# Optimization experiments

Hardware: AMD Instinct MI355X
Metric: run time of the kernel (lower is better)

Reference implementation:

```python
import jax, jax.numpy as jnp
import numpy as np

EMBED_DIM = 400          # d; entity embedding is 2d (alpha|beta)
N_ENTITY = 100000
N_RELATION = 500
HIDDEN = 1600
BATCH = 8192


def _reg(x):
    # Regularizer(base_add=1, min_val=0.05, max_val=1e9)
    return jnp.clip(x + 1.0, 0.05, 1e9)


def setup_inputs() -> dict:
    key = jax.random.key(0)
    ks = jax.random.split(key, 16)
    d = EMBED_DIM
    rng = (9.0 + 2.0) / d  # (gamma + epsilon) / embed_dim with gamma=9

    def xavier(k, shape):
        fan_out, fan_in = shape
        lim = np.sqrt(6.0 / (fan_in + fan_out))
        return jax.random.uniform(k, shape, jnp.float32, -lim, lim)

    inp = {
        "anchor1_idx": jax.random.randint(ks[0], (BATCH,), 0, N_ENTITY),
        "rel1_idx": jax.random.randint(ks[1], (BATCH,), 0, N_RELATION),
        "anchor2_idx": jax.random.randint(ks[2], (BATCH,), 0, N_ENTITY),
        "rel2_idx": jax.random.randint(ks[3], (BATCH,), 0, N_RELATION),
        # embedding tables
        "entity_embedding": jax.random.uniform(ks[4], (N_ENTITY, 2 * d), jnp.float32, -rng, rng),
        "relation_embedding": jax.random.uniform(ks[5], (N_RELATION, d), jnp.float32, -rng, rng),
        # BetaProjection: layer1 [hidden, 2d+d], layer2 [hidden, hidden], layer0 [2d, hidden]
        "pW1": xavier(ks[6], (HIDDEN, 3 * d)),
        "pb1": jnp.zeros((HIDDEN,), jnp.float32),
        "pW2": xavier(ks[7], (HIDDEN, HIDDEN)),
        "pb2": jnp.zeros((HIDDEN,), jnp.float32),
        "pW0": xavier(ks[8], (2 * d, HIDDEN)),
        "pb0": jnp.zeros((2 * d,), jnp.float32),
        # BetaIntersection: layer1 [2d, 2d], layer2 [d, 2d]
        "iW1": xavier(ks[9], (2 * d, 2 * d)),
        "ib1": jnp.zeros((2 * d,), jnp.float32),
        "iW2": xavier(ks[10], (d, 2 * d)),
        "ib2": jnp.zeros((d,), jnp.float32),
    }
    return inp


def _projection(e_emb, r_emb, pW1, pb1, pW2, pb2, pW0, pb0):
    # cat -> Linear+ReLU (layer1) -> Linear+ReLU (layer2) -> layer0 -> regularizer
    x = jnp.concatenate([e_emb, r_emb], axis=-1)           # [B, 3d]
    x = jax.nn.relu(x @ pW1.T + pb1)                       # [B, H]
    x = jax.nn.relu(x @ pW2.T + pb2)                       # [B, H]
    x = x @ pW0.T + pb0                                    # [B, 2d]
    return _reg(x)


def _intersection(alphas, betas, iW1, ib1, iW2, ib2):
    # alphas/betas: [K, B, d]; softmax attention over K
    all_emb = jnp.concatenate([alphas, betas], axis=-1)    # [K, B, 2d]
    h = jax.nn.relu(all_emb @ iW1.T + ib1)                 # [K, B, 2d]
    att = jax.nn.softmax(h @ iW2.T + ib2, axis=0)          # [K, B, d]
    return jnp.sum(att * alphas, axis=0), jnp.sum(att * betas, axis=0)


def reference(anchor1_idx, rel1_idx, anchor2_idx, rel2_idx,
              entity_embedding, relation_embedding,
              pW1, pb1, pW2, pb2, pW0, pb0,
              iW1, ib1, iW2, ib2):
    h = _reg(entity_embedding)                             # entity_regularizer
    r = relation_embedding

    emb1 = _projection(h[anchor1_idx], r[rel1_idx], pW1, pb1, pW2, pb2, pW0, pb0)
    a1, b1 = jnp.split(emb1, 2, axis=-1)
    emb2 = _projection(h[anchor2_idx], r[rel2_idx], pW1, pb1, pW2, pb2, pW0, pb0)
    a2, b2 = jnp.split(emb2, 2, axis=-1)

    alpha, beta = _intersection(jnp.stack([a1, a2]), jnp.stack([b1, b2]),
                                iW1, ib1, iW2, ib2)
    return alpha, beta
```

## Files before the change

kernel.cpp:

```cpp
#include <hip/hip_runtime.h>
#include <hip/hip_bf16.h>
#include <stdint.h>

typedef __bf16 bf16_t;
typedef __bf16 bf16x8 __attribute__((ext_vector_type(8)));
typedef float f32x4 __attribute__((ext_vector_type(4)));

constexpr int BATCH = 8192;
constexpr int M = 2 * BATCH;

constexpr int K1 = 1216;
constexpr int LDC1 = 1664, NS1 = 1600;
constexpr int LDA2 = 1664, KL2 = 1600;
constexpr int LDC2 = 1664, NS2 = 1600;
constexpr int LDA3 = 1664, KL3 = 1600;
constexpr int N3c = 1024;
constexpr int LDC3 = 1024, NS3 = 832;
constexpr int LDA4 = 1024, KL4 = 832;
constexpr int N4c = 1024;
constexpr int LDC4 = 1024, NS4 = 832;
constexpr int LDA5 = 1024, KL5 = 832, N5 = 512;
constexpr int NW1 = 1792, NW2 = 1792;

__device__ __forceinline__ void gload_lds16(const void* g, void* l) {
  __builtin_amdgcn_global_load_lds(
      (const __attribute__((address_space(1))) void*)g,
      (__attribute__((address_space(3))) void*)l,
      16, 0, 0);
}

#define CFENCE() asm volatile("" ::: "memory")
#define BAR()  { CFENCE(); __builtin_amdgcn_s_barrier(); CFENCE(); }

__device__ __forceinline__ void doconv(int idx, const float* __restrict__ src,
                                       bf16_t* __restrict__ dst, int Nr, int Kc, int Kp) {
  const int kp4 = Kp >> 2;
  const int r = idx / kp4;
  const int c = (idx - r * kp4) << 2;
  union { bf16_t h[4]; uint2 u; } pk;
#pragma unroll
  for (int j = 0; j < 4; ++j) {
    const int cc = c + j;
    const float v = (r < Nr && cc < Kc) ? src[(size_t)r * Kc + cc] : 0.f;
    pk.h[j] = (bf16_t)v;
  }
  *(uint2*)(dst + (size_t)r * Kp + c) = pk.u;
}

constexpr int CJ0 = NW1 * K1 / 4;
constexpr int CJ1 = CJ0 + NW2 * LDA2 / 4;
constexpr int CJ2 = CJ1 + N3c * LDA3 / 4;
constexpr int CJ3 = CJ2 + N4c * LDA4 / 4;
constexpr int CJ4 = CJ3 + N5 * LDA5 / 4;
constexpr int GATHERB = 2048;
constexpr int CONVB = 2048;
constexpr int PREPB = GATHERB + CONVB;

__global__ void prep_kernel(const int* __restrict__ a1, const int* __restrict__ r1,
                            const int* __restrict__ a2, const int* __restrict__ r2,
                            const float* __restrict__ ent, const float* __restrict__ rel,
                            bf16_t* __restrict__ X,
                            const float* __restrict__ pW1, const float* __restrict__ pW2,
                            const float* __restrict__ pW0, const float* __restrict__ iW1,
                            const float* __restrict__ iW2,
                            bf16_t* __restrict__ W1b, bf16_t* __restrict__ W2b,
                            bf16_t* __restrict__ W0b, bf16_t* __restrict__ iW1b,
                            bf16_t* __restrict__ iW2b) {
  if (blockIdx.x < GATHERB) {
    for (int r8 = 0; r8 < 8; ++r8) {
      const int row = blockIdx.x * 8 + r8;
      const int b   = row & (BATCH - 1);
      const int br  = row >> 13;
      const int eidx = br ? a2[b] : a1[b];
      const int ridx = br ? r2[b] : r1[b];
      const float* __restrict__ esrc = ent + (size_t)eidx * 800;
      const float* __restrict__ rsrc = rel + (size_t)ridx * 400;
      bf16_t* __restrict__ dst = X + (size_t)row * K1;
      for (int g = threadIdx.x; g < K1 / 4; g += 256) {
        const int c = g * 4;
        float4 v = make_float4(0.f, 0.f, 0.f, 0.f);
        if (c < 800) {
          v = *(const float4*)(esrc + c);
          v.x = fminf(fmaxf(v.x + 1.f, 0.05f), 1e9f);
          v.y = fminf(fmaxf(v.y + 1.f, 0.05f), 1e9f);
          v.z = fminf(fmaxf(v.z + 1.f, 0.05f), 1e9f);
          v.w = fminf(fmaxf(v.w + 1.f, 0.05f), 1e9f);
        } else if (c < 1200) {
          v = *(const float4*)(rsrc + (c - 800));
        }
        union { bf16_t h[4]; uint2 u; } pk;
        pk.h[0] = (bf16_t)v.x; pk.h[1] = (bf16_t)v.y;
        pk.h[2] = (bf16_t)v.z; pk.h[3] = (bf16_t)v.w;
        *(uint2*)(dst + c) = pk.u;
      }
    }
  } else {
    for (int idx = (blockIdx.x - GATHERB) * 256 + threadIdx.x; idx < CJ4;
         idx += CONVB * 256) {
      if (idx < CJ0)      doconv(idx,        pW1, W1b, 1600, 1200, K1);
      else if (idx < CJ1) doconv(idx - CJ0,  pW2, W2b, 1600, 1600, LDA2);
      else if (idx < CJ2) doconv(idx - CJ1,  pW0, W0b,  800, 1600, LDA3);
      else if (idx < CJ3) doconv(idx - CJ2,  iW1, iW1b, 800,  800, LDA4);
      else                doconv(idx - CJ3,  iW2, iW2b, 400,  800, LDA5);
    }
  }
}

enum { ACT_RELU = 0, ACT_REG = 1 };

template <int ACT, int NFR>
__device__ __forceinline__
void gemm_body(const bf16_t* __restrict__ A, const bf16_t* __restrict__ Bw,
               const float* __restrict__ bias, int Nbias, bf16_t* __restrict__ Cb,
               int lda, int Nstore, int ldc, int NT, int bm, int col0,
               bf16_t* ldsbase, int t) {
  const int lane = t & 63;
  const int wv = t >> 6;
  const int wm = wv >> 2, wn = wv & 3;
  const int l15 = lane & 15;
  const int kbs = (((lane >> 4) ^ ((l15 >> 1) & 3)) << 4);

  const int srow = t >> 2;
  const int skc  = (t & 3) ^ ((t >> 3) & 3);
  const bf16_t* aR0 = A  + (size_t)(bm * 256 + srow) * lda + skc * 8;
  const bf16_t* aR1 = aR0 + (size_t)128 * lda;
  const bf16_t* bR0 = Bw + (size_t)(col0 + srow) * lda + skc * 8;
  const bf16_t* bR1 = bR0 + (size_t)128 * lda;
  const int ldsb0 = (wv * 64) * 16;
  const int ldsb1 = (512 + wv * 64) * 16;

  auto SLOT = [&](int s) { return ldsbase + s * 8192; };
  auto STAGE = [&](const bf16_t* r0p, const bf16_t* r1p, int kOff, bf16_t* slot) {
    gload_lds16(r0p + kOff, (char*)slot + ldsb0);
    gload_lds16(r1p + kOff, (char*)slot + ldsb1);
  };

  f32x4 acc[8][NFR];
#pragma unroll
  for (int i = 0; i < 8; ++i)
#pragma unroll
    for (int j = 0; j < NFR; ++j) acc[i][j] = f32x4{0.f, 0.f, 0.f, 0.f};

  STAGE(aR0, aR1, 0, SLOT(0));
  STAGE(bR0, bR1, 0, SLOT(2));
  STAGE(aR0, aR1, 32, SLOT(1));
  STAGE(bR0, bR1, 32, SLOT(3));
  if (NT > 1) {
    STAGE(aR0, aR1, 64, SLOT(4));
    STAGE(bR0, bR1, 64, SLOT(6));
    asm volatile("s_waitcnt vmcnt(8)" ::: "memory");
  } else {
    asm volatile("s_waitcnt vmcnt(4)" ::: "memory");
  }
  __builtin_amdgcn_s_barrier();
  CFENCE();

  bf16x8 bfr[NFR];
  int db = 0;
  for (int kt = 0; kt < NT; ++kt, db ^= 1) {
    const bool p1 = (kt + 1) < NT;
    const bool p2 = (kt + 2) < NT;
    bf16_t* const cur = SLOT(db * 4);
    bf16_t* const nxt = SLOT((db ^ 1) * 4);

    {
      const char* sA = (const char*)(cur);
      const char* sB = (const char*)(cur + 2 * 8192);
      bf16x8 af[4];
#pragma unroll
      for (int i = 0; i < 4; ++i)
        af[i] = *(const bf16x8*)(sA + ((wm * 128 + i * 16 + l15) << 6) + kbs);
#pragma unroll
      for (int i = 0; i < NFR; ++i)
        bfr[i] = *(const bf16x8*)(sB + ((wn * (NFR * 16) + i * 16 + l15) << 6) + kbs);
      if (p1) STAGE(aR0, aR1, (kt + 1) * 64 + 32, nxt + 1 * 8192);
      BAR();
      __builtin_amdgcn_s_setprio(1);
#pragma unroll
      for (int i = 0; i < 4; ++i)
#pragma unroll
        for (int j = 0; j < NFR; ++j)
          acc[i][j] = __builtin_amdgcn_mfma_f32_16x16x32_bf16(af[i], bfr[j], acc[i][j], 0, 0, 0);
      __builtin_amdgcn_s_setprio(0);
      BAR();
    }
    {
      const char* sA = (const char*)(cur);
      bf16x8 af[4];
#pragma unroll
      for (int i = 0; i < 4; ++i)
        af[i] = *(const bf16x8*)(sA + ((wm * 128 + (4 + i) * 16 + l15) << 6) + kbs);
      if (p1) STAGE(bR0, bR1, (kt + 1) * 64 + 32, nxt + 3 * 8192);
      BAR();
      __builtin_amdgcn_s_setprio(1);
#pragma unroll
      for (int i = 0; i < 4; ++i)
#pragma unroll
        for (int j = 0; j < NFR; ++j)
          acc[4 + i][j] = __builtin_amdgcn_mfma_f32_16x16x32_bf16(af[i], bfr[j], acc[4 + i][j], 0, 0, 0);
      __builtin_amdgcn_s_setprio(0);
      if (p1) asm volatile("s_waitcnt vmcnt(8)" ::: "memory");
      else    asm volatile("s_waitcnt vmcnt(0)" ::: "memory");
      BAR();
    }
    {
      const char* sA = (const char*)(cur + 1 * 8192);
      const char* sB = (const char*)(cur + 3 * 8192);
      bf16x8 af[4];
#pragma unroll
      for (int i = 0; i < 4; ++i)
        af[i] = *(const bf16x8*)(sA + ((wm * 128 + i * 16 + l15) << 6) + kbs);
#pragma unroll
      for (int i = 0; i < NFR; ++i)
        bfr[i] = *(const bf16x8*)(sB + ((wn * (NFR * 16) + i * 16 + l15) << 6) + kbs);
      if (p2) STAGE(aR0, aR1, (kt + 2) * 64, cur + 0 * 8192);
      BAR();
      __builtin_amdgcn_s_setprio(1);
#pragma unroll
      for (int i = 0; i < 4; ++i)
#pragma unroll
        for (int j = 0; j < NFR; ++j)
          acc[i][j] = __builtin_amdgcn_mfma_f32_16x16x32_bf16(af[i], bfr[j], acc[i][j], 0, 0, 0);
      __builtin_amdgcn_s_setprio(0);
      BAR();
    }
    {
      const char* sA = (const char*)(cur + 1 * 8192);
      bf16x8 af[4];
#pragma unroll
      for (int i = 0; i < 4; ++i)
        af[i] = *(const bf16x8*)(sA + ((wm * 128 + (4 + i) * 16 + l15) << 6) + kbs);
      if (p2) STAGE(bR0, bR1, (kt + 2) * 64, cur + 2 * 8192);
      BAR();
      __builtin_amdgcn_s_setprio(1);
#pragma unroll
      for (int i = 0; i < 4; ++i)
#pragma unroll
        for (int j = 0; j < NFR; ++j)
          acc[4 + i][j] = __builtin_amdgcn_mfma_f32_16x16x32_bf16(af[i], bfr[j], acc[4 + i][j], 0, 0, 0);
      __builtin_amdgcn_s_setprio(0);
      if (p1) {
        if (p2) asm volatile("s_waitcnt vmcnt(8)" ::: "memory");
        else    asm volatile("s_waitcnt vmcnt(4)" ::: "memory");
      }
      BAR();
    }
  }

  const int r0 = bm * 256 + wm * 128 + ((lane >> 4) * 4);
  const int c0 = col0 + wn * (NFR * 16) + l15;
#pragma unroll
  for (int ni = 0; ni < NFR; ++ni) {
    const int col = c0 + ni * 16;
    const float bv = (col < Nbias) ? bias[col] : 0.f;
    const bool cok = (col < Nstore);
#pragma unroll
    for (int mi = 0; mi < 8; ++mi) {
#pragma unroll
      for (int j = 0; j < 4; ++j) {
        float v = acc[mi][ni][j] + bv;
        if (ACT == ACT_RELU) v = fmaxf(v, 0.f);
        else                 v = fminf(fmaxf(v + 1.f, 0.05f), 1e9f);
        if (cok) Cb[(size_t)(r0 + mi * 16 + j) * ldc + col] = (bf16_t)v;
      }
    }
  }
}

template <int ACT, bool MIXED>
__global__ __launch_bounds__(512)
void gemm256(const bf16_t* __restrict__ A, const bf16_t* __restrict__ Bw,
             const float* __restrict__ bias, int Nbias,
             bf16_t* __restrict__ Cb,
             int lda, int Nstore, int ldc, int NT, int gridN) {
  __shared__ __align__(16) bf16_t lds[8][8192];
  const int nwg = gridDim.x;
  const int id = blockIdx.x;
  const int swz = (id & 7) * (nwg >> 3) + (id >> 3);
  const int bn = swz % gridN, bm = swz / gridN;
  const int t = threadIdx.x;
  if (MIXED) {
    const int col0 = bn * 192;
    if (bn < gridN - 1)
      gemm_body<ACT, 3>(A, Bw, bias, Nbias, Cb, lda, Nstore, ldc, NT, bm, col0, &lds[0][0], t);
    else
      gemm_body<ACT, 4>(A, Bw, bias, Nbias, Cb, lda, Nstore, ldc, NT, bm, col0, &lds[0][0], t);
  } else {
    gemm_body<ACT, 4>(A, Bw, bias, Nbias, Cb, lda, Nstore, ldc, NT, bm, bn * 256, &lds[0][0], t);
  }
}

constexpr int NT5 = KL5 / 64;
__global__ __launch_bounds__(256)
void g5_combine(const bf16_t* __restrict__ H, const bf16_t* __restrict__ Wb,
                const float* __restrict__ ib2, const bf16_t* __restrict__ E,
                float* __restrict__ out) {
  __shared__ __align__(16) bf16_t As1[2][8192];
  __shared__ __align__(16) bf16_t As2[2][8192];
  __shared__ __align__(16) bf16_t Bs[2][8192];

  const int bn = blockIdx.x, bm = blockIdx.y;
  const int t = threadIdx.x;
  const int lane = t & 63;
  const int wv = t >> 6;
  const int wm = wv >> 1, wn = wv & 1;

  f32x4 acc1[4][4], acc2[4][4];
#pragma unroll
  for (int i = 0; i < 4; ++i)
#pragma unroll
    for (int j = 0; j < 4; ++j) { acc1[i][j] = f32x4{0.f,0.f,0.f,0.f}; acc2[i][j] = f32x4{0.f,0.f,0.f,0.f}; }

  const size_t a1Base = (size_t)(bm * 128) * LDA5;
  const size_t a2Base = (size_t)(8192 + bm * 128) * LDA5;
  const size_t bBase  = (size_t)(bn * 128) * LDA5;

  auto stage = [&](int db, int kt) {
#pragma unroll
    for (int q = 0; q < 4; ++q) {
      const int lin = q * 256 + t;
      const int row = lin >> 3;
      const int kc = ((lin & 7) ^ (row & 7)) * 8;
      const int lofs = (q * 256 + wv * 64) * 16;
      gload_lds16(H + a1Base + (size_t)row * LDA5 + kt + kc, (char*)As1[db] + lofs);
      gload_lds16(H + a2Base + (size_t)row * LDA5 + kt + kc, (char*)As2[db] + lofs);
      gload_lds16(Wb + bBase + (size_t)row * LDA5 + kt + kc, (char*)Bs[db] + lofs);
    }
  };

  stage(0, 0);
  __syncthreads();
  int db = 0;
  for (int it = 0; it < NT5; ++it) {
    if (it + 1 < NT5) stage(db ^ 1, (it + 1) * 64);
#pragma unroll
    for (int s = 0; s < 2; ++s) {
      const int crd = s * 4 + (lane >> 4);
      const int k0 = (crd ^ (lane & 7)) * 8;
      bf16x8 af1[4], af2[4], bf[4];
#pragma unroll
      for (int i = 0; i < 4; ++i) {
        const int ra = wm * 64 + i * 16 + (lane & 15);
        af1[i] = *(const bf16x8*)(As1[db] + ra * 64 + k0);
        af2[i] = *(const bf16x8*)(As2[db] + ra * 64 + k0);
        const int rb = wn * 64 + i * 16 + (lane & 15);
        bf[i] = *(const bf16x8*)(Bs[db] + rb * 64 + k0);
      }
#pragma unroll
      for (int mi = 0; mi < 4; ++mi)
#pragma unroll
        for (int ni = 0; ni < 4; ++ni) {
          acc1[mi][ni] = __builtin_amdgcn_mfma_f32_16x16x32_bf16(af1[mi], bf[ni], acc1[mi][ni], 0, 0, 0);
          acc2[mi][ni] = __builtin_amdgcn_mfma_f32_16x16x32_bf16(af2[mi], bf[ni], acc2[mi][ni], 0, 0, 0);
        }
    }
    __syncthreads();
    db ^= 1;
  }

  const int rloc0 = wm * 64 + ((lane >> 4) * 4);
  const int cloc0 = wn * 64 + (lane & 15);
#pragma unroll
  for (int ni = 0; ni < 4; ++ni) {
    const int d = bn * 128 + cloc0 + ni * 16;
    if (d >= 400) continue;
    const float bv = ib2[d];
#pragma unroll
    for (int mi = 0; mi < 4; ++mi) {
#pragma unroll
      for (int j = 0; j < 4; ++j) {
        const int b = bm * 128 + rloc0 + mi * 16 + j;
        const float l1 = acc1[mi][ni][j] + bv;
        const float l2 = acc2[mi][ni][j] + bv;
        const float att1 = 1.f / (1.f + expf(l2 - l1));
        const float att2 = 1.f - att1;
        const bf16_t* E1 = E + (size_t)b * LDC3;
        const bf16_t* E2 = E + (size_t)(8192 + b) * LDC3;
        out[(size_t)b * 400 + d] =
            att1 * (float)E1[d] + att2 * (float)E2[d];
        out[(size_t)8192 * 400 + (size_t)b * 400 + d] =
            att1 * (float)E1[400 + d] + att2 * (float)E2[400 + d];
      }
    }
  }
}

extern "C" void kernel_launch(void* const* d_in, const int* in_sizes, int n_in,
                              void* d_out, int out_size, void* d_ws, size_t ws_size,
                              hipStream_t stream) {
  const int* a1 = (const int*)d_in[0];
  const int* r1 = (const int*)d_in[1];
  const int* a2 = (const int*)d_in[2];
  const int* r2 = (const int*)d_in[3];
  const float* ent = (const float*)d_in[4];
  const float* rel = (const float*)d_in[5];
  const float* pW1 = (const float*)d_in[6];
  const float* pb1 = (const float*)d_in[7];
  const float* pW2 = (const float*)d_in[8];
  const float* pb2 = (const float*)d_in[9];
  const float* pW0 = (const float*)d_in[10];
  const float* pb0 = (const float*)d_in[11];
  const float* iW1 = (const float*)d_in[12];
  const float* ib1 = (const float*)d_in[13];
  const float* iW2 = (const float*)d_in[14];
  const float* ib2 = (const float*)d_in[15];

  char* ws = (char*)d_ws;
  size_t o = 0;
  auto take = [&](size_t bytes) { char* p = ws + o; o += (bytes + 255) & ~(size_t)255; return p; };
  bf16_t* W1b  = (bf16_t*)take((size_t)NW1 * K1 * 2);
  bf16_t* W2b  = (bf16_t*)take((size_t)NW2 * LDA2 * 2);
  bf16_t* W0b  = (bf16_t*)take((size_t)N3c * LDA3 * 2);
  bf16_t* iW1b = (bf16_t*)take((size_t)N4c * LDA4 * 2);
  bf16_t* iW2b = (bf16_t*)take((size_t)N5 * LDA5 * 2);
  char* bufX = take((size_t)M * K1 * 2);
  char* bufY = take((size_t)M * LDC1 * 2);
  char* bufZ = take((size_t)M * LDC2 * 2);

  bf16_t* Xb = (bf16_t*)bufX;
  bf16_t* Yb = (bf16_t*)bufY;
  bf16_t* Zb = (bf16_t*)bufZ;
  bf16_t* Eb = (bf16_t*)bufX;
  bf16_t* Hb = (bf16_t*)bufY;

  prep_kernel<<<dim3(PREPB), 256, 0, stream>>>(a1, r1, a2, r2, ent, rel, Xb,
                                               pW1, pW2, pW0, iW1, iW2,
                                               W1b, W2b, W0b, iW1b, iW2b);

  gemm256<ACT_RELU, true><<<dim3(8 * (M / 256)), 512, 0, stream>>>(
      Xb, W1b, pb1, 1600, Yb, K1, NS1, LDC1, K1 / 64, 8);
  gemm256<ACT_RELU, true><<<dim3(8 * (M / 256)), 512, 0, stream>>>(
      Yb, W2b, pb2, 1600, Zb, LDA2, NS2, LDC2, KL2 / 64, 8);
  gemm256<ACT_REG, false><<<dim3(4 * (M / 256)), 512, 0, stream>>>(
      Zb, W0b, pb0, 800, Eb, LDA3, NS3, LDC3, KL3 / 64, 4);
  gemm256<ACT_RELU, false><<<dim3(4 * (M / 256)), 512, 0, stream>>>(
      Eb, iW1b, ib1, 800, Hb, LDA4, NS4, LDC4, KL4 / 64, 4);
  g5_combine<<<dim3(N5 / 128, BATCH / 128), 256, 0, stream>>>(
      Hb, iW2b, ib2, Eb, (float*)d_out);
}
```

Before: 349.0 us.

## Precompute relation-part of first projection layer as per-relation table

Splits the first projection GEMM into an entity part (K reduced from 1216 to 832) and a relation part. The relation part is computed once per distinct relation (500 rows) by a small GEMM into a table, then added in the epilogue through each row's relation index. The K of the largest-M first layer shrinks by about a third, at the cost of an extra small kernel and gathered bias-like loads in the epilogue. The first and second layer grids are also remapped with a fixed block-to-tile ordering.

```diff
diff --git a/kernel.cpp b/kernel.cpp
--- a/kernel.cpp
+++ b/kernel.cpp
@@ -9,7 +9,7 @@
 constexpr int BATCH = 8192;
 constexpr int M = 2 * BATCH;
 
-constexpr int K1 = 1216;
+constexpr int K1 = 832;
 constexpr int LDC1 = 1664, NS1 = 1600;
 constexpr int LDA2 = 1664, KL2 = 1600;
 constexpr int LDC2 = 1664, NS2 = 1600;
@@ -21,6 +21,8 @@
 constexpr int LDC4 = 1024, NS4 = 832;
 constexpr int LDA5 = 1024, KL5 = 832, N5 = 512;
 constexpr int NW1 = 1792, NW2 = 1792;
+constexpr int KREL = 448;
+constexpr int LDP = 1664;
 
 __device__ __forceinline__ void gload_lds16(const void* g, void* l) {
   __builtin_amdgcn_global_load_lds(
@@ -32,7 +34,7 @@
 #define CFENCE() asm volatile("" ::: "memory")
 #define BAR()  { CFENCE(); __builtin_amdgcn_s_barrier(); CFENCE(); }
 
-__device__ __forceinline__ void doconv(int idx, const float* __restrict__ src,
+__device__ __forceinline__ void doconv(int idx, const float* __restrict__ src, int sstride,
                                        bf16_t* __restrict__ dst, int Nr, int Kc, int Kp) {
   const int kp4 = Kp >> 2;
   const int r = idx / kp4;
@@ -41,7 +43,7 @@
 #pragma unroll
   for (int j = 0; j < 4; ++j) {
     const int cc = c + j;
-    const float v = (r < Nr && cc < Kc) ? src[(size_t)r * Kc + cc] : 0.f;
+    const float v = (r < Nr && cc < Kc) ? src[(size_t)r * sstride + cc] : 0.f;
     pk.h[j] = (bf16_t)v;
   }
   *(uint2*)(dst + (size_t)r * Kp + c) = pk.u;
@@ -52,6 +54,8 @@
 constexpr int CJ2 = CJ1 + N3c * LDA3 / 4;
 constexpr int CJ3 = CJ2 + N4c * LDA4 / 4;
 constexpr int CJ4 = CJ3 + N5 * LDA5 / 4;
+constexpr int CJ5 = CJ4 + LDP * KREL / 4;
+constexpr int CJ6 = CJ5 + 512 * KREL / 4;
 constexpr int GATHERB = 2048;
 constexpr int CONVB = 2048;
 constexpr int PREPB = GATHERB + CONVB;
@@ -59,13 +63,14 @@
 __global__ void prep_kernel(const int* __restrict__ a1, const int* __restrict__ r1,
                             const int* __restrict__ a2, const int* __restrict__ r2,
                             const float* __restrict__ ent, const float* __restrict__ rel,
-                            bf16_t* __restrict__ X,
+                            bf16_t* __restrict__ X, int* __restrict__ relrow,
                             const float* __restrict__ pW1, const float* __restrict__ pW2,
                             const float* __restrict__ pW0, const float* __restrict__ iW1,
                             const float* __restrict__ iW2,
-                            bf16_t* __restrict__ W1b, bf16_t* __restrict__ W2b,
+                            bf16_t* __restrict__ W1a, bf16_t* __restrict__ W2b,
                             bf16_t* __restrict__ W0b, bf16_t* __restrict__ iW1b,
-                            bf16_t* __restrict__ iW2b) {
+                            bf16_t* __restrict__ iW2b, bf16_t* __restrict__ W1bT,
+                            bf16_t* __restrict__ relbf) {
   if (blockIdx.x < GATHERB) {
     for (int r8 = 0; r8 < 8; ++r8) {
       const int row = blockIdx.x * 8 + r8;
@@ -73,8 +78,8 @@
       const int br  = row >> 13;
       const int eidx = br ? a2[b] : a1[b];
       const int ridx = br ? r2[b] : r1[b];
+      if (threadIdx.x == 0) relrow[row] = ridx;
       const float* __restrict__ esrc = ent + (size_t)eidx * 800;
-      const float* __restrict__ rsrc = rel + (size_t)ridx * 400;
       bf16_t* __restrict__ dst = X + (size_t)row * K1;
       for (int g = threadIdx.x; g < K1 / 4; g += 256) {
         const int c = g * 4;
@@ -85,8 +90,6 @@
           v.y = fminf(fmaxf(v.y + 1.f, 0.05f), 1e9f);
           v.z = fminf(fmaxf(v.z + 1.f, 0.05f), 1e9f);
           v.w = fminf(fmaxf(v.w + 1.f, 0.05f), 1e9f);
-        } else if (c < 1200) {
-          v = *(const float4*)(rsrc + (c - 800));
         }
         union { bf16_t h[4]; uint2 u; } pk;
         pk.h[0] = (bf16_t)v.x; pk.h[1] = (bf16_t)v.y;
@@ -95,24 +98,27 @@
       }
     }
   } else {
-    for (int idx = (blockIdx.x - GATHERB) * 256 + threadIdx.x; idx < CJ4;
+    for (int idx = (blockIdx.x - GATHERB) * 256 + threadIdx.x; idx < CJ6;
          idx += CONVB * 256) {
-      if (idx < CJ0)      doconv(idx,        pW1, W1b, 1600, 1200, K1);
-      else if (idx < CJ1) doconv(idx - CJ0,  pW2, W2b, 1600, 1600, LDA2);
-      else if (idx < CJ2) doconv(idx - CJ1,  pW0, W0b,  800, 1600, LDA3);
-      else if (idx < CJ3) doconv(idx - CJ2,  iW1, iW1b, 800,  800, LDA4);
-      else                doconv(idx - CJ3,  iW2, iW2b, 400,  800, LDA5);
-    }
-  }
-}
-
-enum { ACT_RELU = 0, ACT_REG = 1 };
-
-template <int ACT, int NFR>
+      if (idx < CJ0)      doconv(idx,        pW1, 1200, W1a, 1600,  800, K1);
+      else if (idx < CJ1) doconv(idx - CJ0,  pW2, 1600, W2b, 1600, 1600, LDA2);
+      else if (idx < CJ2) doconv(idx - CJ1,  pW0, 1600, W0b,  800, 1600, LDA3);
+      else if (idx < CJ3) doconv(idx - CJ2,  iW1,  800, iW1b, 800,  800, LDA4);
+      else if (idx < CJ4) doconv(idx - CJ3,  iW2,  800, iW2b, 400,  800, LDA5);
+      else if (idx < CJ5) doconv(idx - CJ4,  pW1 + 800, 1200, W1bT, 1600, 400, KREL);
+      else                doconv(idx - CJ5,  rel,  400, relbf, 500, 400, KREL);
+    }
+  }
+}
+
+enum { ACT_RELU = 0, ACT_REG = 1, ACT_NONE = 2 };
+
+template <int ACT, int NFR, bool ROWADD>
 __device__ __forceinline__
 void gemm_body(const bf16_t* __restrict__ A, const bf16_t* __restrict__ Bw,
                const float* __restrict__ bias, int Nbias, bf16_t* __restrict__ Cb,
                int lda, int Nstore, int ldc, int NT, int bm, int col0,
+               const int* __restrict__ relrow, const bf16_t* __restrict__ Pb,
                bf16_t* ldsbase, int t) {
   const int lane = t & 63;
   const int wv = t >> 6;
@@ -249,44 +255,130 @@
 
   const int r0 = bm * 256 + wm * 128 + ((lane >> 4) * 4);
   const int c0 = col0 + wn * (NFR * 16) + l15;
+  float bvv[NFR]; int colv[NFR]; bool cokv[NFR];
 #pragma unroll
   for (int ni = 0; ni < NFR; ++ni) {
-    const int col = c0 + ni * 16;
-    const float bv = (col < Nbias) ? bias[col] : 0.f;
-    const bool cok = (col < Nstore);
-#pragma unroll
-    for (int mi = 0; mi < 8; ++mi) {
-#pragma unroll
-      for (int j = 0; j < 4; ++j) {
-        float v = acc[mi][ni][j] + bv;
+    colv[ni] = c0 + ni * 16;
+    bvv[ni] = (colv[ni] < Nbias) ? bias[colv[ni]] : 0.f;
+    cokv[ni] = (colv[ni] < Nstore);
+  }
+#pragma unroll
+  for (int mi = 0; mi < 8; ++mi) {
+#pragma unroll
+    for (int j = 0; j < 4; ++j) {
+      const int row = r0 + mi * 16 + j;
+      int rr = 0;
+      if (ROWADD) rr = relrow[row];
+#pragma unroll
+      for (int ni = 0; ni < NFR; ++ni) {
+        float v = acc[mi][ni][j] + bvv[ni];
+        if (ROWADD) v += (float)Pb[(size_t)rr * LDP + colv[ni]];
         if (ACT == ACT_RELU) v = fmaxf(v, 0.f);
-        else                 v = fminf(fmaxf(v + 1.f, 0.05f), 1e9f);
-        if (cok) Cb[(size_t)(r0 + mi * 16 + j) * ldc + col] = (bf16_t)v;
-      }
-    }
-  }
-}
-
-template <int ACT, bool MIXED>
+        else if (ACT == ACT_REG) v = fminf(fmaxf(v + 1.f, 0.05f), 1e9f);
+        if (cokv[ni]) Cb[(size_t)row * ldc + colv[ni]] = (bf16_t)v;
+      }
+    }
+  }
+}
+
+template <int ACT, bool MIXED, bool ROWADD>
 __global__ __launch_bounds__(512)
 void gemm256(const bf16_t* __restrict__ A, const bf16_t* __restrict__ Bw,
              const float* __restrict__ bias, int Nbias,
              bf16_t* __restrict__ Cb,
-             int lda, int Nstore, int ldc, int NT, int gridN) {
+             int lda, int Nstore, int ldc, int NT, int gridN,
+             const int* __restrict__ relrow, const bf16_t* __restrict__ Pb) {
   __shared__ __align__(16) bf16_t lds[8][8192];
-  const int nwg = gridDim.x;
   const int id = blockIdx.x;
-  const int swz = (id & 7) * (nwg >> 3) + (id >> 3);
-  const int bn = swz % gridN, bm = swz / gridN;
   const int t = threadIdx.x;
   if (MIXED) {
+    const int r = id >> 8;
+    const int j = id & 255;
+    const int n = (j & 7) * 32 + (j >> 3);
+    const int bm = n >> 2;
+    const int bn = (r == 0) ? (n & 3) : 4 + (n & 3);
     const int col0 = bn * 192;
-    if (bn < gridN - 1)
-      gemm_body<ACT, 3>(A, Bw, bias, Nbias, Cb, lda, Nstore, ldc, NT, bm, col0, &lds[0][0], t);
+    if (bn < 7)
+      gemm_body<ACT, 3, ROWADD>(A, Bw, bias, Nbias, Cb, lda, Nstore, ldc, NT, bm, col0, relrow, Pb, &lds[0][0], t);
     else
-      gemm_body<ACT, 4>(A, Bw, bias, Nbias, Cb, lda, Nstore, ldc, NT, bm, col0, &lds[0][0], t);
+      gemm_body<ACT, 4, ROWADD>(A, Bw, bias, Nbias, Cb, lda, Nstore, ldc, NT, bm, col0, relrow, Pb, &lds[0][0], t);
   } else {
-    gemm_body<ACT, 4>(A, Bw, bias, Nbias, Cb, lda, Nstore, ldc, NT, bm, bn * 256, &lds[0][0], t);
+    const int nwg = gridDim.x;
+    const int swz = (id & 7) * (nwg >> 3) + (id >> 3);
+    const int bn = swz % gridN, bm = swz / gridN;
+    gemm_body<ACT, 4, ROWADD>(A, Bw, bias, Nbias, Cb, lda, Nstore, ldc, NT, bm, bn * 256, relrow, Pb, &lds[0][0], t);
+  }
+}
+
+__global__ __launch_bounds__(256)
+void gemm_kernel(const bf16_t* __restrict__ A, const bf16_t* __restrict__ Bw,
+                 int Nbias, const float* __restrict__ bias,
+                 bf16_t* __restrict__ Cb, int lda, int Kloop, int ldc) {
+  __shared__ __align__(16) bf16_t As[128 * 64];
+  __shared__ __align__(16) bf16_t Bs[128 * 64];
+
+  const int bn = blockIdx.x, bm = blockIdx.y;
+  const int t = threadIdx.x;
+  const int lane = t & 63;
+  const int wv = t >> 6;
+  const int wm = wv >> 1, wn = wv & 1;
+
+  f32x4 acc[4][4];
+#pragma unroll
+  for (int i = 0; i < 4; ++i)
+#pragma unroll
+    for (int j = 0; j < 4; ++j) acc[i][j] = f32x4{0.f, 0.f, 0.f, 0.f};
+
+  const size_t aBase = (size_t)(bm * 128) * lda;
+  const size_t bBase = (size_t)(bn * 128) * lda;
+
+  for (int kt = 0; kt < Kloop; kt += 64) {
+    __syncthreads();
+#pragma unroll
+    for (int q = 0; q < 4; ++q) {
+      const int lin = q * 256 + t;
+      const int row = lin >> 3;
+      const int kc = ((lin & 7) ^ (row & 7)) * 8;
+      const int lofs = (q * 256 + wv * 64) * 16;
+      gload_lds16(A + aBase + (size_t)row * lda + kt + kc, (char*)As + lofs);
+      gload_lds16(Bw + bBase + (size_t)row * lda + kt + kc, (char*)Bs + lofs);
+    }
+    __syncthreads();
+
+#pragma unroll
+    for (int s = 0; s < 2; ++s) {
+      const int crd = s * 4 + (lane >> 4);
+      const int k0 = (crd ^ (lane & 7)) * 8;
+      bf16x8 af[4], bf[4];
+#pragma unroll
+      for (int i = 0; i < 4; ++i) {
+        const int ra = wm * 64 + i * 16 + (lane & 15);
+        af[i] = *(const bf16x8*)(As + ra * 64 + k0);
+        const int rb = wn * 64 + i * 16 + (lane & 15);
+        bf[i] = *(const bf16x8*)(Bs + rb * 64 + k0);
+      }
+#pragma unroll
+      for (int mi = 0; mi < 4; ++mi)
+#pragma unroll
+        for (int ni = 0; ni < 4; ++ni)
+          acc[mi][ni] = __builtin_amdgcn_mfma_f32_16x16x32_bf16(af[mi], bf[ni], acc[mi][ni], 0, 0, 0);
+    }
+  }
+
+  const int r0 = bm * 128 + wm * 64 + ((lane >> 4) * 4);
+  const int c0 = bn * 128 + wn * 64 + (lane & 15);
+#pragma unroll
+  for (int ni = 0; ni < 4; ++ni) {
+    const int col = c0 + ni * 16;
+    const float bv = (col < Nbias) ? bias[col] : 0.f;
+#pragma unroll
+    for (int mi = 0; mi < 4; ++mi) {
+#pragma unroll
+      for (int j = 0; j < 4; ++j) {
+        float v = acc[mi][ni][j] + bv;
+        Cb[(size_t)(r0 + mi * 16 + j) * ldc + col] = (bf16_t)v;
+      }
+    }
   }
 }
 
@@ -408,12 +500,16 @@
   char* ws = (char*)d_ws;
   size_t o = 0;
   auto take = [&](size_t bytes) { char* p = ws + o; o += (bytes + 255) & ~(size_t)255; return p; };
-  bf16_t* W1b  = (bf16_t*)take((size_t)NW1 * K1 * 2);
+  bf16_t* W1a  = (bf16_t*)take((size_t)NW1 * K1 * 2);
   bf16_t* W2b  = (bf16_t*)take((size_t)NW2 * LDA2 * 2);
   bf16_t* W0b  = (bf16_t*)take((size_t)N3c * LDA3 * 2);
   bf16_t* iW1b = (bf16_t*)take((size_t)N4c * LDA4 * 2);
   bf16_t* iW2b = (bf16_t*)take((size_t)N5 * LDA5 * 2);
-  char* bufX = take((size_t)M * K1 * 2);
+  bf16_t* W1bT = (bf16_t*)take((size_t)LDP * KREL * 2);
+  bf16_t* relbf= (bf16_t*)take((size_t)512 * KREL * 2);
+  bf16_t* Pmat = (bf16_t*)take((size_t)512 * LDP * 2);
+  int*    relrow = (int*)take((size_t)M * 4);
+  char* bufX = take((size_t)M * 1024 * 2);
   char* bufY = take((size_t)M * LDC1 * 2);
   char* bufZ = take((size_t)M * LDC2 * 2);
 
@@ -423,18 +519,21 @@
   bf16_t* Eb = (bf16_t*)bufX;
   bf16_t* Hb = (bf16_t*)bufY;
 
-  prep_kernel<<<dim3(PREPB), 256, 0, stream>>>(a1, r1, a2, r2, ent, rel, Xb,
+  prep_kernel<<<dim3(PREPB), 256, 0, stream>>>(a1, r1, a2, r2, ent, rel, Xb, relrow,
                                                pW1, pW2, pW0, iW1, iW2,
-                                               W1b, W2b, W0b, iW1b, iW2b);
-
-  gemm256<ACT_RELU, true><<<dim3(8 * (M / 256)), 512, 0, stream>>>(
-      Xb, W1b, pb1, 1600, Yb, K1, NS1, LDC1, K1 / 64, 8);
-  gemm256<ACT_RELU, true><<<dim3(8 * (M / 256)), 512, 0, stream>>>(
-      Yb, W2b, pb2, 1600, Zb, LDA2, NS2, LDC2, KL2 / 64, 8);
-  gemm256<ACT_REG, false><<<dim3(4 * (M / 256)), 512, 0, stream>>>(
-      Zb, W0b, pb0, 800, Eb, LDA3, NS3, LDC3, KL3 / 64, 4);
-  gemm256<ACT_RELU, false><<<dim3(4 * (M / 256)), 512, 0, stream>>>(
-      Eb, iW1b, ib1, 800, Hb, LDA4, NS4, LDC4, KL4 / 64, 4);
+                                               W1a, W2b, W0b, iW1b, iW2b, W1bT, relbf);
+
+  gemm_kernel<<<dim3(LDP / 128, 512 / 128), 256, 0, stream>>>(
+      relbf, W1bT, 0, pb1, Pmat, KREL, KREL, LDP);
+
+  gemm256<ACT_RELU, true, true><<<dim3(512), 512, 0, stream>>>(
+      Xb, W1a, pb1, 1600, Yb, K1, NS1, LDC1, K1 / 64, 8, relrow, Pmat);
+  gemm256<ACT_RELU, true, false><<<dim3(512), 512, 0, stream>>>(
+      Yb, W2b, pb2, 1600, Zb, LDA2, NS2, LDC2, KL2 / 64, 8, nullptr, nullptr);
+  gemm256<ACT_REG, false, false><<<dim3(256), 512, 0, stream>>>(
+      Zb, W0b, pb0, 800, Eb, LDA3, NS3, LDC3, KL3 / 64, 4, nullptr, nullptr);
+  gemm256<ACT_RELU, false, false><<<dim3(256), 512, 0, stream>>>(
+      Eb, iW1b, ib1, 800, Hb, LDA4, NS4, LDC4, KL4 / 64, 4, nullptr, nullptr);
   g5_combine<<<dim3(N5 / 128, BATCH / 128), 256, 0, stream>>>(
       Hb, iW2b, ib2, Eb, (float*)d_out);
 }
```

Measured after the change: 441.4 us. 26.5% more time.

## Persistent paired-tile GEMM scheduling and one-row-per-block prep gather

Applied to the files above, without the earlier changes.

The first two 1600-wide GEMMs now launch 256 workgroups that each compute two column tiles in sequence. The narrow 192-column tiles are paired so every workgroup gets balanced work, and each XCD is mapped to a fixed set of row blocks. This is meant to remove the tail imbalance of a 512-workgroup grid with mixed tile widths and to improve A-tile reuse within each XCD's L2. The prep kernel now uses one block per gathered row and one thread per weight-conversion chunk, giving more parallelism at the cost of many more blocks.

```diff
diff --git a/kernel.cpp b/kernel.cpp
--- a/kernel.cpp
+++ b/kernel.cpp
@@ -52,9 +52,8 @@
 constexpr int CJ2 = CJ1 + N3c * LDA3 / 4;
 constexpr int CJ3 = CJ2 + N4c * LDA4 / 4;
 constexpr int CJ4 = CJ3 + N5 * LDA5 / 4;
-constexpr int GATHERB = 2048;
-constexpr int CONVB = 2048;
-constexpr int PREPB = GATHERB + CONVB;
+constexpr int CONV_BLOCKS = CJ4 / 256;
+constexpr int PREP_BLOCKS = M + CONV_BLOCKS;
 
 __global__ void prep_kernel(const int* __restrict__ a1, const int* __restrict__ r1,
                             const int* __restrict__ a2, const int* __restrict__ r2,
@@ -66,43 +65,39 @@
                             bf16_t* __restrict__ W1b, bf16_t* __restrict__ W2b,
                             bf16_t* __restrict__ W0b, bf16_t* __restrict__ iW1b,
                             bf16_t* __restrict__ iW2b) {
-  if (blockIdx.x < GATHERB) {
-    for (int r8 = 0; r8 < 8; ++r8) {
-      const int row = blockIdx.x * 8 + r8;
-      const int b   = row & (BATCH - 1);
-      const int br  = row >> 13;
-      const int eidx = br ? a2[b] : a1[b];
-      const int ridx = br ? r2[b] : r1[b];
-      const float* __restrict__ esrc = ent + (size_t)eidx * 800;
-      const float* __restrict__ rsrc = rel + (size_t)ridx * 400;
-      bf16_t* __restrict__ dst = X + (size_t)row * K1;
-      for (int g = threadIdx.x; g < K1 / 4; g += 256) {
-        const int c = g * 4;
-        float4 v = make_float4(0.f, 0.f, 0.f, 0.f);
-        if (c < 800) {
-          v = *(const float4*)(esrc + c);
-          v.x = fminf(fmaxf(v.x + 1.f, 0.05f), 1e9f);
-          v.y = fminf(fmaxf(v.y + 1.f, 0.05f), 1e9f);
-          v.z = fminf(fmaxf(v.z + 1.f, 0.05f), 1e9f);
-          v.w = fminf(fmaxf(v.w + 1.f, 0.05f), 1e9f);
-        } else if (c < 1200) {
-          v = *(const float4*)(rsrc + (c - 800));
-        }
-        union { bf16_t h[4]; uint2 u; } pk;
-        pk.h[0] = (bf16_t)v.x; pk.h[1] = (bf16_t)v.y;
-        pk.h[2] = (bf16_t)v.z; pk.h[3] = (bf16_t)v.w;
-        *(uint2*)(dst + c) = pk.u;
+  if (blockIdx.x < M) {
+    const int row = blockIdx.x;
+    const int b   = row & (BATCH - 1);
+    const int br  = row >> 13;
+    const int eidx = br ? a2[b] : a1[b];
+    const int ridx = br ? r2[b] : r1[b];
+    const float* __restrict__ esrc = ent + (size_t)eidx * 800;
+    const float* __restrict__ rsrc = rel + (size_t)ridx * 400;
+    bf16_t* __restrict__ dst = X + (size_t)row * K1;
+    for (int g = threadIdx.x; g < K1 / 4; g += 256) {
+      const int c = g * 4;
+      float4 v = make_float4(0.f, 0.f, 0.f, 0.f);
+      if (c < 800) {
+        v = *(const float4*)(esrc + c);
+        v.x = fminf(fmaxf(v.x + 1.f, 0.05f), 1e9f);
+        v.y = fminf(fmaxf(v.y + 1.f, 0.05f), 1e9f);
+        v.z = fminf(fmaxf(v.z + 1.f, 0.05f), 1e9f);
+        v.w = fminf(fmaxf(v.w + 1.f, 0.05f), 1e9f);
+      } else if (c < 1200) {
+        v = *(const float4*)(rsrc + (c - 800));
       }
+      union { bf16_t h[4]; uint2 u; } pk;
+      pk.h[0] = (bf16_t)v.x; pk.h[1] = (bf16_t)v.y;
+      pk.h[2] = (bf16_t)v.z; pk.h[3] = (bf16_t)v.w;
+      *(uint2*)(dst + c) = pk.u;
     }
   } else {
-    for (int idx = (blockIdx.x - GATHERB) * 256 + threadIdx.x; idx < CJ4;
-         idx += CONVB * 256) {
-      if (idx < CJ0)      doconv(idx,        pW1, W1b, 1600, 1200, K1);
-      else if (idx < CJ1) doconv(idx - CJ0,  pW2, W2b, 1600, 1600, LDA2);
-      else if (idx < CJ2) doconv(idx - CJ1,  pW0, W0b,  800, 1600, LDA3);
-      else if (idx < CJ3) doconv(idx - CJ2,  iW1, iW1b, 800,  800, LDA4);
-      else                doconv(idx - CJ3,  iW2, iW2b, 400,  800, LDA5);
-    }
+    const int idx = (blockIdx.x - M) * 256 + threadIdx.x;
+    if (idx < CJ0)      doconv(idx,        pW1, W1b, 1600, 1200, K1);
+    else if (idx < CJ1) doconv(idx - CJ0,  pW2, W2b, 1600, 1600, LDA2);
+    else if (idx < CJ2) doconv(idx - CJ1,  pW0, W0b,  800, 1600, LDA3);
+    else if (idx < CJ3) doconv(idx - CJ2,  iW1, iW1b, 800,  800, LDA4);
+    else if (idx < CJ4) doconv(idx - CJ3,  iW2, iW2b, 400,  800, LDA5);
   }
 }
 
@@ -267,27 +262,43 @@
   }
 }
 
-template <int ACT, bool MIXED>
+template <int ACT>
 __global__ __launch_bounds__(512)
-void gemm256(const bf16_t* __restrict__ A, const bf16_t* __restrict__ Bw,
-             const float* __restrict__ bias, int Nbias,
-             bf16_t* __restrict__ Cb,
-             int lda, int Nstore, int ldc, int NT, int gridN) {
+void gemm256_pair(const bf16_t* __restrict__ A, const bf16_t* __restrict__ Bw,
+                  const float* __restrict__ bias, int Nbias,
+                  bf16_t* __restrict__ Cb,
+                  int lda, int Nstore, int ldc, int NT) {
+  __shared__ __align__(16) bf16_t lds[8][8192];
+  const int b = blockIdx.x;
+  const int xcd = b & 7;
+  const int local = b >> 3;
+  const int bm = xcd * 8 + (local & 7);
+  const int s = local >> 3;
+  const int t = threadIdx.x;
+  const int bnA = (s == 0) ? 0 : (2 * s - 1);
+  const int bnB = (s == 0) ? 7 : (2 * s);
+#pragma unroll 1
+  for (int i = 0; i < 2; ++i) {
+    const int bn = i ? bnB : bnA;
+    if (bn < 7)
+      gemm_body<ACT, 3>(A, Bw, bias, Nbias, Cb, lda, Nstore, ldc, NT, bm, bn * 192, &lds[0][0], t);
+    else
+      gemm_body<ACT, 4>(A, Bw, bias, Nbias, Cb, lda, Nstore, ldc, NT, bm, 1344, &lds[0][0], t);
+  }
+}
+
+template <int ACT>
+__global__ __launch_bounds__(512)
+void gemm256u(const bf16_t* __restrict__ A, const bf16_t* __restrict__ Bw,
+              const float* __restrict__ bias, int Nbias,
+              bf16_t* __restrict__ Cb,
+              int lda, int Nstore, int ldc, int NT, int gridN) {
   __shared__ __align__(16) bf16_t lds[8][8192];
   const int nwg = gridDim.x;
   const int id = blockIdx.x;
   const int swz = (id & 7) * (nwg >> 3) + (id >> 3);
   const int bn = swz % gridN, bm = swz / gridN;
-  const int t = threadIdx.x;
-  if (MIXED) {
-    const int col0 = bn * 192;
-    if (bn < gridN - 1)
-      gemm_body<ACT, 3>(A, Bw, bias, Nbias, Cb, lda, Nstore, ldc, NT, bm, col0, &lds[0][0], t);
-    else
-      gemm_body<ACT, 4>(A, Bw, bias, Nbias, Cb, lda, Nstore, ldc, NT, bm, col0, &lds[0][0], t);
-  } else {
-    gemm_body<ACT, 4>(A, Bw, bias, Nbias, Cb, lda, Nstore, ldc, NT, bm, bn * 256, &lds[0][0], t);
-  }
+  gemm_body<ACT, 4>(A, Bw, bias, Nbias, Cb, lda, Nstore, ldc, NT, bm, bn * 256, &lds[0][0], threadIdx.x);
 }
 
 constexpr int NT5 = KL5 / 64;
@@ -369,16 +380,16 @@
     for (int mi = 0; mi < 4; ++mi) {
 #pragma unroll
       for (int j = 0; j < 4; ++j) {
-        const int b = bm * 128 + rloc0 + mi * 16 + j;
+        const int b2 = bm * 128 + rloc0 + mi * 16 + j;
         const float l1 = acc1[mi][ni][j] + bv;
         const float l2 = acc2[mi][ni][j] + bv;
         const float att1 = 1.f / (1.f + expf(l2 - l1));
         const float att2 = 1.f - att1;
-        const bf16_t* E1 = E + (size_t)b * LDC3;
-        const bf16_t* E2 = E + (size_t)(8192 + b) * LDC3;
-        out[(size_t)b * 400 + d] =
+        const bf16_t* E1 = E + (size_t)b2 * LDC3;
+        const bf16_t* E2 = E + (size_t)(8192 + b2) * LDC3;
+        out[(size_t)b2 * 400 + d] =
             att1 * (float)E1[d] + att2 * (float)E2[d];
-        out[(size_t)8192 * 400 + (size_t)b * 400 + d] =
+        out[(size_t)8192 * 400 + (size_t)b2 * 400 + d] =
             att1 * (float)E1[400 + d] + att2 * (float)E2[400 + d];
       }
     }
@@ -423,17 +434,17 @@
   bf16_t* Eb = (bf16_t*)bufX;
   bf16_t* Hb = (bf16_t*)bufY;
 
-  prep_kernel<<<dim3(PREPB), 256, 0, stream>>>(a1, r1, a2, r2, ent, rel, Xb,
-                                               pW1, pW2, pW0, iW1, iW2,
-                                               W1b, W2b, W0b, iW1b, iW2b);
-
-  gemm256<ACT_RELU, true><<<dim3(8 * (M / 256)), 512, 0, stream>>>(
-      Xb, W1b, pb1, 1600, Yb, K1, NS1, LDC1, K1 / 64, 8);
-  gemm256<ACT_RELU, true><<<dim3(8 * (M / 256)), 512, 0, stream>>>(
-      Yb, W2b, pb2, 1600, Zb, LDA2, NS2, LDC2, KL2 / 64, 8);
-  gemm256<ACT_REG, false><<<dim3(4 * (M / 256)), 512, 0, stream>>>(
+  prep_kernel<<<dim3(PREP_BLOCKS), 256, 0, stream>>>(a1, r1, a2, r2, ent, rel, Xb,
+                                                     pW1, pW2, pW0, iW1, iW2,
+                                                     W1b, W2b, W0b, iW1b, iW2b);
+
+  gemm256_pair<ACT_RELU><<<dim3(256), 512, 0, stream>>>(
+      Xb, W1b, pb1, 1600, Yb, K1, NS1, LDC1, K1 / 64);
+  gemm256_pair<ACT_RELU><<<dim3(256), 512, 0, stream>>>(
+      Yb, W2b, pb2, 1600, Zb, LDA2, NS2, LDC2, KL2 / 64);
+  gemm256u<ACT_REG><<<dim3(256), 512, 0, stream>>>(
       Zb, W0b, pb0, 800, Eb, LDA3, NS3, LDC3, KL3 / 64, 4);
-  gemm256<ACT_RELU, false><<<dim3(4 * (M / 256)), 512, 0, stream>>>(
+  gemm256u<ACT_RELU><<<dim3(256), 512, 0, stream>>>(
       Eb, iW1b, ib1, 800, Hb, LDA4, NS4, LDC4, KL4 / 64, 4);
   g5_combine<<<dim3(N5 / 128, BATCH / 128), 256, 0, stream>>>(
       Hb, iW2b, ib2, Eb, (float*)d_out);
```

After: 515.2 us. 47.6% more time.
